# Performance work log

Hardware: AMD Instinct MI355X
Metric: run time of the kernel (lower is better)

Reference implementation:

```python
import jax, jax.numpy as jnp
import numpy as np


def _gcn_norm(edge_index, num_nodes):
    # PyG GCNConv(normalize=True): add self-loops, symmetric normalization.
    src, dst = edge_index[0], edge_index[1]
    loop = jnp.arange(num_nodes, dtype=src.dtype)
    src = jnp.concatenate([src, loop])
    dst = jnp.concatenate([dst, loop])
    ones = jnp.ones(src.shape[0], dtype=jnp.float32)
    deg = jax.ops.segment_sum(ones, dst, num_segments=num_nodes)
    dinv = jax.lax.rsqrt(jnp.maximum(deg, 1.0))  # deg >= 1 with self-loops
    norm = dinv[src] * dinv[dst]  # [E+N]
    return src, dst, norm


def _gcn_layer(x, W, b, src, dst, norm, num_nodes):
    h = x @ W                                   # [N, out]
    msg = norm[:, None] * h[src]                # [E+N, out] gather
    agg = jax.ops.segment_sum(msg, dst, num_segments=num_nodes)  # scatter-add
    return agg + b


def setup_inputs() -> dict:
    key = jax.random.key(0)
    ks = jax.random.split(key, 8)
    N, E, F = 50000, 400000, 128
    v = jax.random.normal(ks[0], (N, F), dtype=jnp.float32)
    edge_index = jax.random.randint(ks[1], (2, E), 0, N, dtype=jnp.int64)
    def glorot(k, fan_in, fan_out):
        s = jnp.sqrt(6.0 / (fan_in + fan_out))
        return jax.random.uniform(k, (fan_in, fan_out), jnp.float32, -s, s)
    return {
        "v": v,
        "edge_index": edge_index,
        "W1": glorot(ks[2], F, 128), "b1": jnp.zeros((128,), jnp.float32),
        "W2": glorot(ks[3], 128, 256), "b2": jnp.zeros((256,), jnp.float32),
        "W3": glorot(ks[4], 256, 512), "b3": jnp.zeros((512,), jnp.float32),
    }


def reference(v, edge_index, W1, b1, W2, b2, W3, b3):
    N = v.shape[0]
    src, dst, norm = _gcn_norm(edge_index, N)
    x = jax.nn.relu(_gcn_layer(v, W1, b1, src, dst, norm, N))
    x = jax.nn.relu(_gcn_layer(x, W2, b2, src, dst, norm, N))
    x = jax.nn.relu(_gcn_layer(x, W3, b3, src, dst, norm, N))
    return x
```

## Files before the change

kernel.cpp:

```cpp
#include <hip/hip_runtime.h>
#include <hip/hip_bf16.h>
#include <stdint.h>

static constexpr int NN = 50000;
static constexpr int NE = 400000;
static constexpr int NB = (NN + 1023) / 1024;

typedef __attribute__((ext_vector_type(8))) short bf16x8;
typedef __attribute__((ext_vector_type(4))) float f32x4;

__device__ inline ushort f2bf(float f) {
    __hip_bfloat16 b = __float2bfloat16(f);
    return *reinterpret_cast<ushort*>(&b);
}
__device__ inline float bfu2f(ushort u) {
    unsigned x = (unsigned)u << 16;
    return __builtin_bit_cast(float, x);
}

__device__ __forceinline__ void gload16(const void* g, void* l) {
    __builtin_amdgcn_global_load_lds(
        (const __attribute__((address_space(1))) void*)g,
        (__attribute__((address_space(3))) void*)l, 16, 0, 0);
}


__global__ void k_count(const int* __restrict__ ei, unsigned* __restrict__ cnt) {
    int e = blockIdx.x * blockDim.x + threadIdx.x;
    if (e < NE) atomicAdd(&cnt[ei[NE + e]], 1u);
}

__global__ void k_dinv(const unsigned* __restrict__ cnt, float* __restrict__ dinv) {
    int i = blockIdx.x * blockDim.x + threadIdx.x;
    if (i < NN) dinv[i] = rsqrtf((float)(cnt[i] + 1u));
}


__global__ __launch_bounds__(1024) void k_scan1(const unsigned* __restrict__ cnt,
                                                unsigned* __restrict__ offs,
                                                unsigned* __restrict__ bsum) {
    __shared__ unsigned sh[1024];
    int i = blockIdx.x * 1024 + (int)threadIdx.x;
    unsigned v = (i < NN) ? cnt[i] : 0u;
    sh[threadIdx.x] = v;
    __syncthreads();
    #pragma unroll
    for (int off = 1; off < 1024; off <<= 1) {
        unsigned add = (threadIdx.x >= (unsigned)off) ? sh[threadIdx.x - off] : 0u;
        __syncthreads();
        sh[threadIdx.x] += add;
        __syncthreads();
    }
    if (i < NN) offs[i] = sh[threadIdx.x] - v;
    if (threadIdx.x == 1023) bsum[blockIdx.x] = sh[1023];
}

__global__ void k_scan2(const unsigned* __restrict__ bsum, unsigned* __restrict__ boff,
                        unsigned* __restrict__ offs) {
    if (threadIdx.x == 0) {
        unsigned acc = 0;
        for (int b = 0; b < NB; ++b) { boff[b] = acc; acc += bsum[b]; }
        offs[NN] = acc;
    }
}

__global__ __launch_bounds__(1024) void k_scan3(unsigned* __restrict__ offs,
                                                const unsigned* __restrict__ boff) {
    int i = blockIdx.x * 1024 + (int)threadIdx.x;
    if (i < NN) offs[i] += boff[blockIdx.x];
}

__global__ void k_fill(const int* __restrict__ ei, const unsigned* __restrict__ offs,
                       unsigned* __restrict__ cursor, const float* __restrict__ dinv,
                       unsigned* __restrict__ csr_src, float* __restrict__ csr_w) {
    int e = blockIdx.x * blockDim.x + threadIdx.x;
    if (e < NE) {
        int s = ei[e];
        int d = ei[NE + e];
        unsigned pos = offs[d] + atomicAdd(&cursor[d], 1u);
        csr_src[pos] = (unsigned)s;
        csr_w[pos] = dinv[s] * dinv[d];
    }
}


__global__ void k_castW(const float* __restrict__ W, ushort* __restrict__ Wt, int K, int N) {
    int i = blockIdx.x * 256 + (int)threadIdx.x;
    if (i >= K * N) return;
    int k = i / N, n = i - k * N;
    Wt[n * K + k] = f2bf(W[i]);
}


__global__ void k_castV(const float* __restrict__ v, ushort* __restrict__ vb, int n4) {
    int i = blockIdx.x * 256 + (int)threadIdx.x;
    if (i >= n4) return;
    float4 f = *reinterpret_cast<const float4*>(v + (size_t)i * 4);
    *reinterpret_cast<ushort4*>(vb + (size_t)i * 4) =
        make_ushort4(f2bf(f.x), f2bf(f.y), f2bf(f.z), f2bf(f.w));
}


template <int VEC>
__global__ __launch_bounds__(256) void k_aggregate(
        const ushort* __restrict__ x, ushort* __restrict__ y,
        const unsigned* __restrict__ offs, const unsigned* __restrict__ csr_src,
        const float* __restrict__ csr_w, const float* __restrict__ dinv) {
    const int F = 64 * VEC;
    int node = blockIdx.x * 4 + ((int)threadIdx.x >> 6);
    int lane = (int)threadIdx.x & 63;
    if (node >= NN) return;

    float di = dinv[node];
    float sw = di * di;
    float acc[VEC];
    const ushort* xs = x + (size_t)node * F + lane * VEC;
    #pragma unroll
    for (int j = 0; j < VEC; ++j) acc[j] = sw * bfu2f(xs[j]);

    auto ld = [&](unsigned s, ushort* u) {
        const ushort* xr = x + (size_t)s * F + lane * VEC;
        if constexpr (VEC == 2)
            *reinterpret_cast<ushort2*>(u) = *reinterpret_cast<const ushort2*>(xr);
        else
            *reinterpret_cast<ushort4*>(u) = *reinterpret_cast<const ushort4*>(xr);
    };

    unsigned beg = offs[node], end = offs[node + 1];
    unsigned idx = beg;
    for (; idx + 3 < end; idx += 4) {
        unsigned s0 = csr_src[idx], s1 = csr_src[idx + 1];
        unsigned s2 = csr_src[idx + 2], s3 = csr_src[idx + 3];
        float w0 = csr_w[idx], w1 = csr_w[idx + 1];
        float w2 = csr_w[idx + 2], w3 = csr_w[idx + 3];
        ushort u0[VEC], u1[VEC], u2[VEC], u3[VEC];
        ld(s0, u0); ld(s1, u1); ld(s2, u2); ld(s3, u3);
        #pragma unroll
        for (int j = 0; j < VEC; ++j) {
            acc[j] = fmaf(w0, bfu2f(u0[j]), acc[j]);
            acc[j] = fmaf(w1, bfu2f(u1[j]), acc[j]);
            acc[j] = fmaf(w2, bfu2f(u2[j]), acc[j]);
            acc[j] = fmaf(w3, bfu2f(u3[j]), acc[j]);
        }
    }
    for (; idx < end; ++idx) {
        unsigned s0 = csr_src[idx];
        float w0 = csr_w[idx];
        ushort u0[VEC];
        ld(s0, u0);
        #pragma unroll
        for (int j = 0; j < VEC; ++j) acc[j] = fmaf(w0, bfu2f(u0[j]), acc[j]);
    }

    size_t ybase = (size_t)node * F + lane * VEC;
    ushort h[VEC];
    #pragma unroll
    for (int j = 0; j < VEC; ++j) h[j] = f2bf(acc[j]);
    if constexpr (VEC == 2) {
        *reinterpret_cast<ushort2*>(y + ybase) = make_ushort2(h[0], h[1]);
    } else {
        *reinterpret_cast<ushort4*>(y + ybase) = make_ushort4(h[0], h[1], h[2], h[3]);
    }
}


template <int NT, int SC, bool OUTB>
__global__ __launch_bounds__(256, 3) void k_gemm6(
        const ushort* __restrict__ Ah, const ushort* __restrict__ Wt,
        const float* __restrict__ bias, void* __restrict__ Cout, int M, int N) {
    constexpr int K = NT * 32;
    constexpr int CHT = (NT > 4) ? 4 : NT;
    constexpr int NCH = NT / CHT;
    __shared__ __align__(16) float smem[8192];
    short* sB = (short*)smem;

    int nwg = (int)gridDim.x;
    int bid = (int)blockIdx.x;
    int q = nwg >> 3, r = nwg & 7;
    int xcd = bid & 7, seq = bid >> 3;
    int swz = (xcd < r ? xcd * (q + 1) : r * (q + 1) + (xcd - r) * q) + seq;
    int bx = swz % SC, by = swz / SC;
    int col0 = bx * 128, row0 = by * 128;

    int tid = (int)threadIdx.x;
    int w = tid >> 6, lane = tid & 63;
    int wr = w >> 1, wc = w & 1;
    int r16 = lane & 15, kg = lane >> 4;

    size_t aoff[4];
    #pragma unroll
    for (int mi = 0; mi < 4; ++mi) {
        int row = row0 + wr * 64 + mi * 16 + r16;
        if (row >= M) row = M - 1;
        aoff[mi] = (size_t)row * K + kg * 8;
    }

    f32x4 acc[4][4] = {};
    bf16x8 ah[3][4];

    #pragma unroll
    for (int mi = 0; mi < 4; ++mi)
        ah[0][mi] = *reinterpret_cast<const bf16x8*>(Ah + aoff[mi]);
    if constexpr (NT > 1) {
        #pragma unroll
        for (int mi = 0; mi < 4; ++mi)
            ah[1][mi] = *reinterpret_cast<const bf16x8*>(Ah + aoff[mi] + 32);
    }

    #pragma unroll
    for (int kc = 0; kc < NCH; ++kc) {
        if (kc) __syncthreads();
        #pragma unroll
        for (int i = 0; i < CHT * 2; ++i) {
            int c = i * 256 + tid;
            int tl = c >> 9, ckg = (c >> 7) & 3, n = c & 127;
            gload16(Wt + (size_t)(col0 + n) * K + (kc * CHT + tl) * 32 + ckg * 8,
                    sB + c * 8);
        }
        __syncthreads();

        #pragma unroll
        for (int t = 0; t < CHT; ++t) {
            const int tg = kc * CHT + t;
            const int cur = tg % 3;
            if (tg + 2 < NT) {
                const int nxt = (tg + 2) % 3;
                #pragma unroll
                for (int mi = 0; mi < 4; ++mi)
                    ah[nxt][mi] = *reinterpret_cast<const bf16x8*>(Ah + aoff[mi] + (tg + 2) * 32);
            }
            bf16x8 bb[4];
            #pragma unroll
            for (int ni = 0; ni < 4; ++ni)
                bb[ni] = *reinterpret_cast<const bf16x8*>(
                    sB + ((t * 4 + kg) * 128 + wc * 64 + ni * 16 + r16) * 8);
            #pragma unroll
            for (int ni = 0; ni < 4; ++ni)
                #pragma unroll
                for (int mi = 0; mi < 4; ++mi)
                    acc[mi][ni] = __builtin_amdgcn_mfma_f32_16x16x32_bf16(ah[cur][mi], bb[ni], acc[mi][ni], 0, 0, 0);
        }
    }

    __syncthreads();
    float* ep = smem + w * (16 * 68);
    int crow0 = (lane >> 4) * 4;
    int ccol = lane & 15;
    int rb = row0 + wr * 64;
    int cb = col0 + wc * 64;
    int rl0 = lane >> 4;
    int cl = (lane & 15) * 4;
    float4 bv = *reinterpret_cast<const float4*>(&bias[cb + cl]);
    #pragma unroll
    for (int mi = 0; mi < 4; ++mi) {
        #pragma unroll
        for (int ni = 0; ni < 4; ++ni)
            #pragma unroll
            for (int j = 0; j < 4; ++j)
                ep[(crow0 + j) * 68 + ni * 16 + ccol] = acc[mi][ni][j];
        #pragma unroll
        for (int s = 0; s < 4; ++s) {
            int rl = s * 4 + rl0;
            int row = rb + mi * 16 + rl;
            if (row < M) {
                float4 vv = *reinterpret_cast<const float4*>(ep + rl * 68 + cl);
                float4 o;
                o.x = fmaxf(vv.x + bv.x, 0.f);
                o.y = fmaxf(vv.y + bv.y, 0.f);
                o.z = fmaxf(vv.z + bv.z, 0.f);
                o.w = fmaxf(vv.w + bv.w, 0.f);
                if constexpr (OUTB) {
                    *reinterpret_cast<ushort4*>((ushort*)Cout + (size_t)row * N + cb + cl) =
                        make_ushort4(f2bf(o.x), f2bf(o.y), f2bf(o.z), f2bf(o.w));
                } else {
                    *reinterpret_cast<float4*>((float*)Cout + (size_t)row * N + cb + cl) = o;
                }
            }
        }
    }
}


extern "C" void kernel_launch(void* const* d_in, const int* in_sizes, int n_in,
                              void* d_out, int out_size, void* d_ws, size_t ws_size,
                              hipStream_t stream) {
    const float* v  = (const float*)d_in[0];
    const int* ei   = (const int*)d_in[1];
    const float* W1 = (const float*)d_in[2];
    const float* b1 = (const float*)d_in[3];
    const float* W2 = (const float*)d_in[4];
    const float* b2 = (const float*)d_in[5];
    const float* W3 = (const float*)d_in[6];
    const float* b3 = (const float*)d_in[7];
    float* out = (float*)d_out;

    char* ws = (char*)d_ws;
    size_t off = 0;
    auto alloc = [&](size_t bytes) {
        void* p = ws + off;
        off = (off + bytes + 255) & ~(size_t)255;
        return p;
    };
    unsigned* cnt    = (unsigned*)(ws + 0);
    unsigned* cursor = (unsigned*)(ws + (size_t)NN * 4);
    ushort* Wt1 = (ushort*)ws;
    ushort* Wt2 = Wt1 + 128 * 128;
    off = ((size_t)NN * 8 + 255) & ~(size_t)255;
    unsigned* offs    = (unsigned*)alloc((size_t)(NN + 1) * 4);
    float*    dinv    = (float*)alloc((size_t)NN * 4);
    unsigned* bsum    = (unsigned*)alloc((size_t)NB * 4);
    unsigned* boff    = (unsigned*)alloc((size_t)NB * 4);
    unsigned* csr_src = (unsigned*)alloc((size_t)NE * 4);
    float*    csr_w   = (float*)alloc((size_t)NE * 4);
    ushort* Wt3 = (ushort*)csr_src;
    ushort* aggA = (ushort*)alloc((size_t)NN * 256 * 2);
    ushort* vb   = (ushort*)alloc((size_t)NN * 128 * 2);
    ushort* xb   = (ushort*)alloc((size_t)NN * 256 * 2);

    hipMemsetAsync(cnt, 0, (size_t)NN * 8, stream);

    k_count<<<(NE + 255) / 256, 256, 0, stream>>>(ei, cnt);
    k_dinv<<<(NN + 255) / 256, 256, 0, stream>>>(cnt, dinv);
    k_scan1<<<NB, 1024, 0, stream>>>(cnt, offs, bsum);
    k_scan2<<<1, 64, 0, stream>>>(bsum, boff, offs);
    k_scan3<<<NB, 1024, 0, stream>>>(offs, boff);
    k_fill<<<(NE + 255) / 256, 256, 0, stream>>>(ei, offs, cursor, dinv, csr_src, csr_w);

    k_castW<<<(128 * 128 + 255) / 256, 256, 0, stream>>>(W1, Wt1, 128, 128);
    k_castW<<<(128 * 256 + 255) / 256, 256, 0, stream>>>(W2, Wt2, 128, 256);
    k_castV<<<(NN * 128 / 4 + 255) / 256, 256, 0, stream>>>(v, vb, NN * 128 / 4);

    int aggGrid = (NN + 3) / 4;
    int gr = (NN + 127) / 128;

    k_aggregate<2><<<aggGrid, 256, 0, stream>>>(vb, aggA, offs, csr_src, csr_w, dinv);
    k_gemm6<4, 1, true><<<gr * 1, 256, 0, stream>>>(aggA, Wt1, b1, xb, NN, 128);

    k_aggregate<2><<<aggGrid, 256, 0, stream>>>(xb, aggA, offs, csr_src, csr_w, dinv);
    k_gemm6<4, 2, true><<<gr * 2, 256, 0, stream>>>(aggA, Wt2, b2, xb, NN, 256);

    k_aggregate<4><<<aggGrid, 256, 0, stream>>>(xb, aggA, offs, csr_src, csr_w, dinv);
    k_castW<<<(256 * 512 + 255) / 256, 256, 0, stream>>>(W3, Wt3, 256, 512);
    k_gemm6<8, 4, false><<<gr * 4, 256, 0, stream>>>(aggA, Wt3, b3, out, NN, 512);
}
```

Baseline: 244.5 us.

## Split aggregation edges across half-waves and shrink GEMM LDS chunking

The aggregation kernel now splits each node's edge list between two half-waves. Each lane loads twice as many features per row with wider vector loads, and the two halves are combined with a cross-lane shuffle before the store. The GEMM lowers its B chunk size so the shared buffer shrinks, and raises the occupancy hint to 4 blocks per CU. The final fp32 output is written with nontemporal stores to avoid polluting the cache. The risks are extra shuffle work, and more chunk iterations with possibly more syncs in the GEMM.

```diff
diff --git a/kernel.cpp b/kernel.cpp
--- a/kernel.cpp
+++ b/kernel.cpp
@@ -7,6 +7,7 @@
 static constexpr int NB = (NN + 1023) / 1024;
 
 typedef __attribute__((ext_vector_type(8))) short bf16x8;
+typedef __attribute__((ext_vector_type(8))) unsigned short u16x8;
 typedef __attribute__((ext_vector_type(4))) float f32x4;
 
 __device__ inline ushort f2bf(float f) {
@@ -107,71 +108,77 @@
         const unsigned* __restrict__ offs, const unsigned* __restrict__ csr_src,
         const float* __restrict__ csr_w, const float* __restrict__ dinv) {
     const int F = 64 * VEC;
+    const int PL = 2 * VEC;
     int node = blockIdx.x * 4 + ((int)threadIdx.x >> 6);
     int lane = (int)threadIdx.x & 63;
     if (node >= NN) return;
+    int h = lane >> 5;
+    int sl = lane & 31;
+
+    auto ld = [&](const ushort* p, ushort* u) {
+        if constexpr (VEC == 2)
+            *reinterpret_cast<ushort4*>(u) = *reinterpret_cast<const ushort4*>(p);
+        else
+            *reinterpret_cast<u16x8*>(u) = *reinterpret_cast<const u16x8*>(p);
+    };
 
     float di = dinv[node];
-    float sw = di * di;
-    float acc[VEC];
-    const ushort* xs = x + (size_t)node * F + lane * VEC;
-    #pragma unroll
-    for (int j = 0; j < VEC; ++j) acc[j] = sw * bfu2f(xs[j]);
-
-    auto ld = [&](unsigned s, ushort* u) {
-        const ushort* xr = x + (size_t)s * F + lane * VEC;
-        if constexpr (VEC == 2)
-            *reinterpret_cast<ushort2*>(u) = *reinterpret_cast<const ushort2*>(xr);
-        else
-            *reinterpret_cast<ushort4*>(u) = *reinterpret_cast<const ushort4*>(xr);
-    };
+    float sw = (h == 0) ? di * di : 0.f;
+    float acc[PL];
+    {
+        ushort u[PL];
+        ld(x + (size_t)node * F + sl * PL, u);
+        #pragma unroll
+        for (int j = 0; j < PL; ++j) acc[j] = sw * bfu2f(u[j]);
+    }
 
     unsigned beg = offs[node], end = offs[node + 1];
-    unsigned idx = beg;
-    for (; idx + 3 < end; idx += 4) {
-        unsigned s0 = csr_src[idx], s1 = csr_src[idx + 1];
-        unsigned s2 = csr_src[idx + 2], s3 = csr_src[idx + 3];
-        float w0 = csr_w[idx], w1 = csr_w[idx + 1];
-        float w2 = csr_w[idx + 2], w3 = csr_w[idx + 3];
-        ushort u0[VEC], u1[VEC], u2[VEC], u3[VEC];
-        ld(s0, u0); ld(s1, u1); ld(s2, u2); ld(s3, u3);
-        #pragma unroll
-        for (int j = 0; j < VEC; ++j) {
+    unsigned e = beg + h;
+    for (; e + 2 < end; e += 4) {
+        unsigned s0 = csr_src[e], s1 = csr_src[e + 2];
+        float w0 = csr_w[e], w1 = csr_w[e + 2];
+        ushort u0[PL], u1[PL];
+        ld(x + (size_t)s0 * F + sl * PL, u0);
+        ld(x + (size_t)s1 * F + sl * PL, u1);
+        #pragma unroll
+        for (int j = 0; j < PL; ++j) {
             acc[j] = fmaf(w0, bfu2f(u0[j]), acc[j]);
             acc[j] = fmaf(w1, bfu2f(u1[j]), acc[j]);
-            acc[j] = fmaf(w2, bfu2f(u2[j]), acc[j]);
-            acc[j] = fmaf(w3, bfu2f(u3[j]), acc[j]);
         }
     }
-    for (; idx < end; ++idx) {
-        unsigned s0 = csr_src[idx];
-        float w0 = csr_w[idx];
-        ushort u0[VEC];
-        ld(s0, u0);
-        #pragma unroll
-        for (int j = 0; j < VEC; ++j) acc[j] = fmaf(w0, bfu2f(u0[j]), acc[j]);
-    }
-
-    size_t ybase = (size_t)node * F + lane * VEC;
-    ushort h[VEC];
-    #pragma unroll
-    for (int j = 0; j < VEC; ++j) h[j] = f2bf(acc[j]);
-    if constexpr (VEC == 2) {
-        *reinterpret_cast<ushort2*>(y + ybase) = make_ushort2(h[0], h[1]);
-    } else {
-        *reinterpret_cast<ushort4*>(y + ybase) = make_ushort4(h[0], h[1], h[2], h[3]);
+    if (e < end) {
+        unsigned s0 = csr_src[e];
+        float w0 = csr_w[e];
+        ushort u0[PL];
+        ld(x + (size_t)s0 * F + sl * PL, u0);
+        #pragma unroll
+        for (int j = 0; j < PL; ++j) acc[j] = fmaf(w0, bfu2f(u0[j]), acc[j]);
+    }
+
+    #pragma unroll
+    for (int j = 0; j < PL; ++j) acc[j] += __shfl_xor(acc[j], 32);
+
+    if (h == 0) {
+        ushort hh[PL];
+        #pragma unroll
+        for (int j = 0; j < PL; ++j) hh[j] = f2bf(acc[j]);
+        ushort* yp = y + (size_t)node * F + sl * PL;
+        if constexpr (VEC == 2)
+            *reinterpret_cast<ushort4*>(yp) = *reinterpret_cast<ushort4*>(hh);
+        else
+            *reinterpret_cast<u16x8*>(yp) = *reinterpret_cast<u16x8*>(hh);
     }
 }
 
 
 template <int NT, int SC, bool OUTB>
-__global__ __launch_bounds__(256, 3) void k_gemm6(
+__global__ __launch_bounds__(256, 4) void k_gemm7(
         const ushort* __restrict__ Ah, const ushort* __restrict__ Wt,
         const float* __restrict__ bias, void* __restrict__ Cout, int M, int N) {
     constexpr int K = NT * 32;
-    constexpr int CHT = (NT > 4) ? 4 : NT;
+    constexpr int CHT = (NT > 2) ? 2 : NT;
     constexpr int NCH = NT / CHT;
-    __shared__ __align__(16) float smem[8192];
+    __shared__ __align__(16) float smem[4352];
     short* sB = (short*)smem;
 
     int nwg = (int)gridDim.x;
@@ -273,7 +280,9 @@
                     *reinterpret_cast<ushort4*>((ushort*)Cout + (size_t)row * N + cb + cl) =
                         make_ushort4(f2bf(o.x), f2bf(o.y), f2bf(o.z), f2bf(o.w));
                 } else {
-                    *reinterpret_cast<float4*>((float*)Cout + (size_t)row * N + cb + cl) = o;
+                    f32x4 ov = {o.x, o.y, o.z, o.w};
+                    __builtin_nontemporal_store(
+                        ov, reinterpret_cast<f32x4*>((float*)Cout + (size_t)row * N + cb + cl));
                 }
             }
         }
@@ -334,12 +343,12 @@
     int gr = (NN + 127) / 128;
 
     k_aggregate<2><<<aggGrid, 256, 0, stream>>>(vb, aggA, offs, csr_src, csr_w, dinv);
-    k_gemm6<4, 1, true><<<gr * 1, 256, 0, stream>>>(aggA, Wt1, b1, xb, NN, 128);
+    k_gemm7<4, 1, true><<<gr * 1, 256, 0, stream>>>(aggA, Wt1, b1, xb, NN, 128);
 
     k_aggregate<2><<<aggGrid, 256, 0, stream>>>(xb, aggA, offs, csr_src, csr_w, dinv);
-    k_gemm6<4, 2, true><<<gr * 2, 256, 0, stream>>>(aggA, Wt2, b2, xb, NN, 256);
+    k_gemm7<4, 2, true><<<gr * 2, 256, 0, stream>>>(aggA, Wt2, b2, xb, NN, 256);
 
     k_aggregate<4><<<aggGrid, 256, 0, stream>>>(xb, aggA, offs, csr_src, csr_w, dinv);
     k_castW<<<(256 * 512 + 255) / 256, 256, 0, stream>>>(W3, Wt3, 256, 512);
-    k_gemm6<8, 4, false><<<gr * 4, 256, 0, stream>>>(aggA, Wt3, b3, out, NN, 512);
-}
+    k_gemm7<8, 4, false><<<gr * 4, 256, 0, stream>>>(aggA, Wt3, b3, out, NN, 512);
+}
```

Result: faster. 238.6 us (-2.4%).
